# Performance work log

Measured on AMD Instinct MI355X. Metric: run time of the kernel, lower is better.

The kernel has to match this reference:

```python
import jax, jax.numpy as jnp
import numpy as np

B, S, D, H, DFF = 4, 2048, 1024, 8, 4096
DH = D // H  # 128
EPS = 1e-5


def layernorm(x, gamma, beta):
    mu = jnp.mean(x, axis=-1, keepdims=True)
    var = jnp.mean(jnp.square(x - mu), axis=-1, keepdims=True)
    return (x - mu) * jax.lax.rsqrt(var + EPS) * gamma + beta


def setup_inputs() -> dict:
    key = jax.random.key(0)
    ks = jax.random.split(key, 6)
    s = 0.02
    return {
        "src": jax.random.normal(ks[0], (B, S, D), jnp.float32),
        "w_qkv": jax.random.normal(ks[1], (D, 3 * D), jnp.float32) * s,
        "w_out": jax.random.normal(ks[2], (D, D), jnp.float32) * s,
        "w1": jax.random.normal(ks[3], (D, DFF), jnp.float32) * s,
        "b1": jnp.zeros((DFF,), jnp.float32),
        "w2": jax.random.normal(ks[4], (DFF, D), jnp.float32) * s,
        "b2": jnp.zeros((D,), jnp.float32),
        "g1": jnp.ones((D,), jnp.float32),
        "beta1": jnp.zeros((D,), jnp.float32),
        "g2": jnp.ones((D,), jnp.float32),
        "beta2": jnp.zeros((D,), jnp.float32),
    }


def reference(src, w_qkv, w_out, w1, b1, w2, b2, g1, beta1, g2, beta2):
    b, s, d = src.shape
    # --- RingAttention == exact causal MHA on a single device ---
    qkv = src @ w_qkv  # [b, s, 3d]
    q, k, v = jnp.split(qkv, 3, axis=-1)
    to_heads = lambda x: x.reshape(b, s, H, DH).transpose(0, 2, 1, 3)  # [b,h,s,dh]
    q, k, v = to_heads(q), to_heads(k), to_heads(v)
    scale = 1.0 / jnp.sqrt(jnp.asarray(DH, src.dtype))
    scores = jnp.einsum('bhqd,bhkd->bhqk', q, k) * scale  # [b,h,s,s]
    causal = jnp.tril(jnp.ones((s, s), bool))
    neg = jnp.asarray(jnp.finfo(src.dtype).min, src.dtype)
    scores = jnp.where(causal, scores, neg)
    attn = jax.nn.softmax(scores, axis=-1)
    o = jnp.einsum('bhqk,bhkd->bhqd', attn, v)  # [b,h,s,dh]
    o = o.transpose(0, 2, 1, 3).reshape(b, s, d) @ w_out
    # dropout layers are identity at inference
    x = layernorm(src + o, g1, beta1)
    ff = jax.nn.relu(x @ w1 + b1) @ w2 + b2
    return layernorm(x + ff, g2, beta2)
```

## Files before the change

### kernel.cpp

```cpp
#include <hip/hip_runtime.h>

typedef unsigned short u16;
typedef __attribute__((ext_vector_type(8))) short short8;
typedef __attribute__((ext_vector_type(4))) float float4v;

#define MFMA_BF16(a, b, c) __builtin_amdgcn_mfma_f32_16x16x32_bf16((a), (b), (c), 0, 0, 0)

#define B_ 4
#define S_ 2048
#define D_ 1024
#define H_ 8
#define DH_ 128
#define DFF_ 4096
#define EPS_ 1e-5f
#define ROWS_ (B_ * S_)
#define CSCALE_ 0.12751672939502f

__device__ __forceinline__ u16 f2bf(float f) {
  union { float f; unsigned u; } x; x.f = f;
  unsigned r = x.u + 0x7fffu + ((x.u >> 16) & 1u);
  return (u16)(r >> 16);
}

typedef __attribute__((address_space(1))) const unsigned int guint;
typedef __attribute__((address_space(3))) unsigned int luint;
__device__ __forceinline__ void gl2lds16(const u16* g, u16* l) {
  __builtin_amdgcn_global_load_lds((guint*)g, (luint*)l, 16, 0, 0);
}

__global__ void cast_bf16_kernel(const float* __restrict__ in, u16* __restrict__ out, int n4) {
  int i = blockIdx.x * blockDim.x + threadIdx.x;
  int stride = gridDim.x * blockDim.x;
  for (; i < n4; i += stride) {
    float4 v = ((const float4*)in)[i];
    ushort4 u;
    u.x = f2bf(v.x); u.y = f2bf(v.y); u.z = f2bf(v.z); u.w = f2bf(v.w);
    ((ushort4*)out)[i] = u;
  }
}

__global__ void transpose_cast_kernel(const float* __restrict__ in, u16* __restrict__ out,
                                      int K, int N) {
  __shared__ float t[32][33];
  int k0 = blockIdx.x * 32, n0 = blockIdx.y * 32;
  int tx = threadIdx.x & 31, ty = threadIdx.x >> 5;
  #pragma unroll
  for (int i = 0; i < 4; ++i)
    t[ty + 8 * i][tx] = in[(size_t)(k0 + ty + 8 * i) * N + n0 + tx];
  __syncthreads();
  #pragma unroll
  for (int i = 0; i < 4; ++i)
    out[(size_t)(n0 + ty + 8 * i) * K + k0 + tx] = f2bf(t[tx][ty + 8 * i]);
}

__global__ void transpose_v_kernel(const u16* __restrict__ in, u16* __restrict__ out) {
  __shared__ u16 t[32][33];
  int s0 = blockIdx.x * 32, d0 = blockIdx.y * 32, bh = blockIdx.z;
  const u16* src = in + (size_t)bh * S_ * DH_;
  u16* dst = out + (size_t)bh * DH_ * S_;
  int tx = threadIdx.x & 31, ty = threadIdx.x >> 5;
  #pragma unroll
  for (int i = 0; i < 4; ++i)
    t[ty + 8 * i][tx] = src[(size_t)(s0 + ty + 8 * i) * DH_ + d0 + tx];
  __syncthreads();
  #pragma unroll
  for (int i = 0; i < 4; ++i)
    dst[(size_t)(d0 + ty + 8 * i) * S_ + s0 + tx] = t[tx][ty + 8 * i];
}

template <int MODE, int KT>
__global__ __launch_bounds__(256) void gemm_kernel(
    const u16* __restrict__ A, const u16* __restrict__ Bt,
    const int M, const int N,
    float* __restrict__ outF, u16* __restrict__ outH, const float* __restrict__ bias,
    const float* __restrict__ resid,
    u16* __restrict__ qo, u16* __restrict__ ko, u16* __restrict__ vo) {
  __shared__ u16 As[2][128][32];
  __shared__ u16 Bs[2][128][32];
  const int tid = threadIdx.x;
  const int lane = tid & 63, wave = tid >> 6;
  const int quad = lane >> 4, r16 = lane & 15;
  const int wm = (wave >> 1) * 64, wn = (wave & 1) * 64;
  const int m0 = blockIdx.x * 128, n0 = blockIdx.y * 128;
  constexpr int K = KT, niter = KT >> 5;

  float4v acc[4][4];
  #pragma unroll
  for (int i = 0; i < 4; ++i)
    #pragma unroll
    for (int j = 0; j < 4; ++j) acc[i][j] = (float4v)0.0f;

  const int drow = lane >> 2;
  const int dchunk = (lane & 3) ^ ((drow ^ (drow >> 2)) & 3);
  const u16* Ag0 = A + (size_t)(m0 + wave * 32 + drow) * K + dchunk * 8;
  const u16* Ag1 = Ag0 + (size_t)16 * K;
  const u16* Bg0 = Bt + (size_t)(n0 + wave * 32 + drow) * K + dchunk * 8;
  const u16* Bg1 = Bg0 + (size_t)16 * K;
  u16* Al0 = &As[0][wave * 32][0];
  u16* Al1 = &As[0][wave * 32 + 16][0];
  u16* Bl0 = &Bs[0][wave * 32][0];
  u16* Bl1 = &Bs[0][wave * 32 + 16][0];
  constexpr int bufStep = 128 * 32;

  const int fcol = (quad ^ ((r16 ^ (r16 >> 2)) & 3)) * 8;

  gl2lds16(Ag0, Al0);
  gl2lds16(Ag1, Al1);
  gl2lds16(Bg0, Bl0);
  gl2lds16(Bg1, Bl1);

  #pragma unroll 2
  for (int i = 0; i < niter; ++i) {
    __syncthreads();
    if (i + 1 < niter) {
      const int k1 = (i + 1) << 5;
      const int bo = ((i + 1) & 1) ? bufStep : 0;
      gl2lds16(Ag0 + k1, Al0 + bo);
      gl2lds16(Ag1 + k1, Al1 + bo);
      gl2lds16(Bg0 + k1, Bl0 + bo);
      gl2lds16(Bg1 + k1, Bl1 + bo);
    }
    const u16* ab = &As[i & 1][0][0];
    const u16* bb = &Bs[i & 1][0][0];
    short8 af[4], bfv[4];
    #pragma unroll
    for (int t = 0; t < 4; ++t)
      af[t] = *(const short8*)(ab + ((wm + t * 16 + r16) << 5) + fcol);
    #pragma unroll
    for (int t = 0; t < 4; ++t)
      bfv[t] = *(const short8*)(bb + ((wn + t * 16 + r16) << 5) + fcol);
    #pragma unroll
    for (int ii = 0; ii < 4; ++ii)
      #pragma unroll
      for (int j = 0; j < 4; ++j) acc[ii][j] = MFMA_BF16(af[ii], bfv[j], acc[ii][j]);
  }

  #pragma unroll
  for (int i = 0; i < 4; ++i) {
    const int rowb = m0 + wm + i * 16 + quad * 4;
    #pragma unroll
    for (int j = 0; j < 4; ++j) {
      const int col = n0 + wn + j * 16 + r16;
      #pragma unroll
      for (int rg = 0; rg < 4; ++rg) {
        float val = acc[i][j][rg];
        const int r = rowb + rg;
        if (MODE == 0) {
          const int part = col >> 10, cc = col & 1023;
          const int h = cc >> 7, dh = cc & 127;
          const int b = r >> 11, s = r & 2047;
          u16* dst = (part == 0) ? qo : (part == 1) ? ko : vo;
          if (part == 0) val *= CSCALE_;
          dst[((size_t)(b * H_ + h) * S_ + s) * DH_ + dh] = f2bf(val);
        } else if (MODE == 1) {
          val += resid[(size_t)r * N + col];
          outF[(size_t)r * N + col] = val;
        } else if (MODE == 2) {
          val += bias[col];
          val = fmaxf(val, 0.0f);
          outH[(size_t)r * N + col] = f2bf(val);
        } else {
          val += bias[col] + resid[(size_t)r * N + col];
          outF[(size_t)r * N + col] = val;
        }
      }
    }
  }
}

__global__ __launch_bounds__(256) void attn_kernel(
    const u16* __restrict__ Q, const u16* __restrict__ Kg,
    const u16* __restrict__ Vtg, u16* __restrict__ O) {
  __shared__ u16 Ks[64][136];
  __shared__ u16 Vt[128][72];
  __shared__ u16 Pw[4][16][72];
  const int tid = threadIdx.x;
  const int lane = tid & 63, wave = tid >> 6;
  const int quad = lane >> 4, r16 = lane & 15;
  const int pairIdx = blockIdx.x;
  const int bh = blockIdx.y;
  const size_t base = (size_t)bh * S_ * DH_;
  const size_t vtb = (size_t)bh * DH_ * S_;
  const int b = bh >> 3, h = bh & 7;

  const u16* kg0 = Kg + base + (size_t)(tid >> 4) * DH_ + (tid & 15) * 8;
  u16* ksl = &Ks[tid >> 4][(tid & 15) * 8];
  const u16* vg0 = Vtg + vtb + (size_t)(tid >> 3) * S_ + (tid & 7) * 8;
  u16* vtl = &Vt[tid >> 3][(tid & 7) * 8];

  for (int half = 0; half < 2; ++half) {
    const int qb = (half == 0) ? pairIdx : 31 - pairIdx;
    const int qr = qb * 64 + wave * 16 + r16;

    short8 aq[4];
    #pragma unroll
    for (int ks = 0; ks < 4; ++ks)
      aq[ks] = *(const short8*)(Q + base + (size_t)qr * DH_ + ks * 32 + quad * 8);

    float4v acco[8];
    #pragma unroll
    for (int i = 0; i < 8; ++i) acco[i] = (float4v)0.0f;
    float m_q = -1e30f, l_q = 0.0f;

    for (int kb = 0; kb <= qb; ++kb) {
      __syncthreads();
      #pragma unroll
      for (int i = 0; i < 4; ++i)
        *(short8*)(ksl + i * 16 * 136) =
            *(const short8*)(kg0 + (size_t)(kb * 64 + i * 16) * DH_);
      #pragma unroll
      for (int i = 0; i < 4; ++i)
        *(short8*)(vtl + i * 32 * 72) =
            *(const short8*)(vg0 + (size_t)i * 32 * S_ + kb * 64);
      __syncthreads();

      float4v accs[4];
      #pragma unroll
      for (int t = 0; t < 4; ++t) accs[t] = (float4v)0.0f;
      #pragma unroll
      for (int ks = 0; ks < 4; ++ks) {
        #pragma unroll
        for (int t = 0; t < 4; ++t) {
          short8 ak = *(const short8*)&Ks[t * 16 + r16][ks * 32 + quad * 8];
          accs[t] = MFMA_BF16(ak, aq[ks], accs[t]);
        }
      }
      if (kb == qb) {
        #pragma unroll
        for (int t = 0; t < 4; ++t)
          #pragma unroll
          for (int rg = 0; rg < 4; ++rg) {
            int kc = kb * 64 + t * 16 + quad * 4 + rg;
            if (kc > qr) accs[t][rg] = -1e30f;
          }
      }
      float mv = accs[0][0];
      #pragma unroll
      for (int t = 0; t < 4; ++t)
        #pragma unroll
        for (int rg = 0; rg < 4; ++rg) mv = fmaxf(mv, accs[t][rg]);
      mv = fmaxf(mv, __shfl_xor(mv, 16));
      mv = fmaxf(mv, __shfl_xor(mv, 32));
      const float mnew = fmaxf(m_q, mv);
      const float alpha = __builtin_amdgcn_exp2f(m_q - mnew);
      float s0 = 0.0f;
      #pragma unroll
      for (int t = 0; t < 4; ++t)
        #pragma unroll
        for (int rg = 0; rg < 4; ++rg) {
          float p = __builtin_amdgcn_exp2f(accs[t][rg] - mnew);
          accs[t][rg] = p;
          s0 += p;
        }
      s0 += __shfl_xor(s0, 16);
      s0 += __shfl_xor(s0, 32);
      l_q = l_q * alpha + s0;
      m_q = mnew;

      #pragma unroll
      for (int t = 0; t < 4; ++t) {
        union { float f; unsigned u; } c0, c1, c2, c3;
        c0.f = accs[t][0]; c1.f = accs[t][1]; c2.f = accs[t][2]; c3.f = accs[t][3];
        uint2 pk;
        pk.x = ((c0.u + 0x8000u) >> 16) | ((c1.u + 0x8000u) & 0xffff0000u);
        pk.y = ((c2.u + 0x8000u) >> 16) | ((c3.u + 0x8000u) & 0xffff0000u);
        *(uint2*)&Pw[wave][r16][t * 16 + quad * 4] = pk;
      }
      float al[4];
      #pragma unroll
      for (int rg = 0; rg < 4; ++rg) al[rg] = __shfl(alpha, quad * 4 + rg);
      #pragma unroll
      for (int nt = 0; nt < 8; ++nt)
        #pragma unroll
        for (int rg = 0; rg < 4; ++rg) acco[nt][rg] *= al[rg];
      asm volatile("s_waitcnt lgkmcnt(0)" ::: "memory");
      #pragma unroll
      for (int ks2 = 0; ks2 < 2; ++ks2) {
        short8 ap = *(const short8*)&Pw[wave][r16][ks2 * 32 + quad * 8];
        #pragma unroll
        for (int nt = 0; nt < 8; ++nt) {
          short8 bv = *(const short8*)&Vt[nt * 16 + r16][ks2 * 32 + quad * 8];
          acco[nt] = MFMA_BF16(ap, bv, acco[nt]);
        }
      }
    }

    float lr[4];
    #pragma unroll
    for (int rg = 0; rg < 4; ++rg) lr[rg] = __shfl(l_q, quad * 4 + rg);
    const int sbase = qb * 64 + wave * 16 + quad * 4;
    #pragma unroll
    for (int nt = 0; nt < 8; ++nt)
      #pragma unroll
      for (int rg = 0; rg < 4; ++rg) {
        float val = acco[nt][rg] / lr[rg];
        O[((size_t)(b * S_ + sbase + rg)) * D_ + h * DH_ + nt * 16 + r16] = f2bf(val);
      }
  }
}

__global__ __launch_bounds__(256) void ln_kernel(
    const float* __restrict__ a,
    const float* __restrict__ g, const float* __restrict__ be,
    float* __restrict__ xf, u16* __restrict__ xb) {
  __shared__ float red[8];
  const int row = blockIdx.x, tid = threadIdx.x;
  float4 v = ((const float4*)(a + (size_t)row * D_))[tid];
  float s = v.x + v.y + v.z + v.w;
  float q = v.x * v.x + v.y * v.y + v.z * v.z + v.w * v.w;
  #pragma unroll
  for (int m = 1; m < 64; m <<= 1) {
    s += __shfl_xor(s, m);
    q += __shfl_xor(q, m);
  }
  const int wave = tid >> 6, lane = tid & 63;
  if (lane == 0) { red[wave] = s; red[4 + wave] = q; }
  __syncthreads();
  s = red[0] + red[1] + red[2] + red[3];
  q = red[4] + red[5] + red[6] + red[7];
  const float mu = s * (1.0f / D_);
  const float var = q * (1.0f / D_) - mu * mu;
  const float inv = rsqrtf(var + EPS_);
  const float4 gg = ((const float4*)g)[tid];
  const float4 bb = ((const float4*)be)[tid];
  float4 y;
  y.x = (v.x - mu) * inv * gg.x + bb.x;
  y.y = (v.y - mu) * inv * gg.y + bb.y;
  y.z = (v.z - mu) * inv * gg.z + bb.z;
  y.w = (v.w - mu) * inv * gg.w + bb.w;
  if (xf) ((float4*)(xf + (size_t)row * D_))[tid] = y;
  if (xb) {
    ushort4 u;
    u.x = f2bf(y.x); u.y = f2bf(y.y); u.z = f2bf(y.z); u.w = f2bf(y.w);
    ((ushort4*)(xb + (size_t)row * D_))[tid] = u;
  }
}

extern "C" void kernel_launch(void* const* d_in, const int* in_sizes, int n_in,
                              void* d_out, int out_size, void* d_ws, size_t ws_size,
                              hipStream_t stream) {
  const float* src   = (const float*)d_in[0];
  const float* w_qkv = (const float*)d_in[1];
  const float* w_out = (const float*)d_in[2];
  const float* w1    = (const float*)d_in[3];
  const float* b1    = (const float*)d_in[4];
  const float* w2    = (const float*)d_in[5];
  const float* b2    = (const float*)d_in[6];
  const float* g1    = (const float*)d_in[7];
  const float* be1   = (const float*)d_in[8];
  const float* g2    = (const float*)d_in[9];
  const float* be2   = (const float*)d_in[10];
  float* out = (float*)d_out;

  char* ws = (char*)d_ws;
  size_t off = 0;
  auto alloc = [&](size_t bytes) -> void* {
    void* p = ws + off;
    off += (bytes + 255) & ~(size_t)255;
    return p;
  };
  u16* src_bf = (u16*)alloc((size_t)ROWS_ * D_ * 2);
  u16* wqkvT  = (u16*)alloc((size_t)3 * D_ * D_ * 2);
  u16* woutT  = (u16*)alloc((size_t)D_ * D_ * 2);
  u16* w1T    = (u16*)alloc((size_t)DFF_ * D_ * 2);
  u16* w2T    = (u16*)alloc((size_t)D_ * DFF_ * 2);
  u16* qbuf   = (u16*)alloc((size_t)ROWS_ * D_ * 2);
  u16* kbuf   = (u16*)alloc((size_t)ROWS_ * D_ * 2);
  u16* vbuf   = (u16*)alloc((size_t)ROWS_ * D_ * 2);
  u16* obuf   = (u16*)alloc((size_t)ROWS_ * D_ * 2);
  u16* vT     = (u16*)alloc((size_t)ROWS_ * D_ * 2);
  float* proj = (float*)alloc((size_t)ROWS_ * D_ * 4);
  float* xf   = (float*)alloc((size_t)ROWS_ * D_ * 4);
  u16* xb     = (u16*)alloc((size_t)ROWS_ * D_ * 2);
  u16* h1     = qbuf;
  float* ff   = proj;

  cast_bf16_kernel<<<2048, 256, 0, stream>>>(src, src_bf, ROWS_ * D_ / 4);
  transpose_cast_kernel<<<dim3(D_ / 32, 3 * D_ / 32), 256, 0, stream>>>(w_qkv, wqkvT, D_, 3 * D_);
  transpose_cast_kernel<<<dim3(D_ / 32, D_ / 32), 256, 0, stream>>>(w_out, woutT, D_, D_);
  transpose_cast_kernel<<<dim3(D_ / 32, DFF_ / 32), 256, 0, stream>>>(w1, w1T, D_, DFF_);
  transpose_cast_kernel<<<dim3(DFF_ / 32, D_ / 32), 256, 0, stream>>>(w2, w2T, DFF_, D_);

  gemm_kernel<0, 1024><<<dim3(ROWS_ / 128, 3 * D_ / 128), 256, 0, stream>>>(
      src_bf, wqkvT, ROWS_, 3 * D_, nullptr, nullptr, nullptr, nullptr, qbuf, kbuf, vbuf);
  transpose_v_kernel<<<dim3(S_ / 32, DH_ / 32, B_ * H_), 256, 0, stream>>>(vbuf, vT);
  attn_kernel<<<dim3(16, B_ * H_), 256, 0, stream>>>(qbuf, kbuf, vT, obuf);
  gemm_kernel<1, 1024><<<dim3(ROWS_ / 128, D_ / 128), 256, 0, stream>>>(
      obuf, woutT, ROWS_, D_, proj, nullptr, nullptr, src, nullptr, nullptr, nullptr);
  ln_kernel<<<ROWS_, 256, 0, stream>>>(proj, g1, be1, xf, xb);
  gemm_kernel<2, 1024><<<dim3(ROWS_ / 128, DFF_ / 128), 256, 0, stream>>>(
      xb, w1T, ROWS_, DFF_, nullptr, h1, b1, nullptr, nullptr, nullptr, nullptr);
  gemm_kernel<3, 4096><<<dim3(ROWS_ / 128, D_ / 128), 256, 0, stream>>>(
      h1, w2T, ROWS_, D_, ff, nullptr, b2, xf, nullptr, nullptr, nullptr);
  ln_kernel<<<ROWS_, 256, 0, stream>>>(ff, g2, be2, out, nullptr);
}
```

Measured before the change: 557.6 us.

## Store GEMM A operands in 128x32 tiled layout and load fragments directly to registers

Every producer of a GEMM A operand (src cast, attention output, LayerNorm bf16 output, FFN1 output) now writes in a tiled 128x32 block layout. The GEMM then reads A fragments straight from global memory into registers, prefetching one k-step ahead, and drops the A shared-memory staging. This removes the A LDS traffic and its swizzle, at the cost of per-lane 16-byte global loads whose latency may not be hidden and of scattered stores in the producer kernels. A is no longer shared through LDS across the two waves that use the same rows, so each A tile is fetched from global or L2 twice.

```diff
diff --git a/kernel.cpp b/kernel.cpp
--- a/kernel.cpp
+++ b/kernel.cpp
@@ -28,15 +28,19 @@
   __builtin_amdgcn_global_load_lds((guint*)g, (luint*)l, 16, 0, 0);
 }
 
-__global__ void cast_bf16_kernel(const float* __restrict__ in, u16* __restrict__ out, int n4) {
-  int i = blockIdx.x * blockDim.x + threadIdx.x;
-  int stride = gridDim.x * blockDim.x;
-  for (; i < n4; i += stride) {
-    float4 v = ((const float4*)in)[i];
-    ushort4 u;
-    u.x = f2bf(v.x); u.y = f2bf(v.y); u.z = f2bf(v.z); u.w = f2bf(v.w);
-    ((ushort4*)out)[i] = u;
-  }
+__device__ __forceinline__ size_t tiled_off(int row, int k, int Kdim) {
+  return ((size_t)(row >> 7) * (Kdim >> 5) + (k >> 5)) * 4096 +
+         (size_t)((row & 127) << 5) + (k & 31);
+}
+
+__global__ void cast_tiled_kernel(const float* __restrict__ in, u16* __restrict__ out) {
+  int idx = blockIdx.x * 256 + threadIdx.x;
+  int g = idx * 4;
+  int m = g >> 10, k = g & 1023;
+  float4 v = *(const float4*)(in + (size_t)g);
+  ushort4 u;
+  u.x = f2bf(v.x); u.y = f2bf(v.y); u.z = f2bf(v.z); u.w = f2bf(v.w);
+  *(ushort4*)(out + tiled_off(m, k, D_)) = u;
 }
 
 __global__ void transpose_cast_kernel(const float* __restrict__ in, u16* __restrict__ out,
@@ -75,7 +79,6 @@
     float* __restrict__ outF, u16* __restrict__ outH, const float* __restrict__ bias,
     const float* __restrict__ resid,
     u16* __restrict__ qo, u16* __restrict__ ko, u16* __restrict__ vo) {
-  __shared__ u16 As[2][128][32];
   __shared__ u16 Bs[2][128][32];
   const int tid = threadIdx.x;
   const int lane = tid & 63, wave = tid >> 6;
@@ -90,24 +93,24 @@
     #pragma unroll
     for (int j = 0; j < 4; ++j) acc[i][j] = (float4v)0.0f;
 
-  const int drow = lane >> 2;
-  const int dchunk = (lane & 3) ^ ((drow ^ (drow >> 2)) & 3);
-  const u16* Ag0 = A + (size_t)(m0 + wave * 32 + drow) * K + dchunk * 8;
-  const u16* Ag1 = Ag0 + (size_t)16 * K;
-  const u16* Bg0 = Bt + (size_t)(n0 + wave * 32 + drow) * K + dchunk * 8;
+  const int drow = lane >> 2, dseg = lane & 3;
+  const u16* Bg0 = Bt + (size_t)(n0 + wave * 32 + drow) * K + dseg * 8;
   const u16* Bg1 = Bg0 + (size_t)16 * K;
-  u16* Al0 = &As[0][wave * 32][0];
-  u16* Al1 = &As[0][wave * 32 + 16][0];
   u16* Bl0 = &Bs[0][wave * 32][0];
   u16* Bl1 = &Bs[0][wave * 32 + 16][0];
   constexpr int bufStep = 128 * 32;
 
-  const int fcol = (quad ^ ((r16 ^ (r16 >> 2)) & 3)) * 8;
-
-  gl2lds16(Ag0, Al0);
-  gl2lds16(Ag1, Al1);
+  const u16* ap[4];
+  #pragma unroll
+  for (int t = 0; t < 4; ++t)
+    ap[t] = A + (size_t)(m0 >> 7) * niter * 4096 +
+            (size_t)((wm + t * 16 + r16) << 5) + quad * 8;
+
   gl2lds16(Bg0, Bl0);
   gl2lds16(Bg1, Bl1);
+  short8 a_cur[4], a_nxt[4];
+  #pragma unroll
+  for (int t = 0; t < 4; ++t) a_cur[t] = *(const short8*)(ap[t]);
 
   #pragma unroll 2
   for (int i = 0; i < niter; ++i) {
@@ -115,24 +118,22 @@
     if (i + 1 < niter) {
       const int k1 = (i + 1) << 5;
       const int bo = ((i + 1) & 1) ? bufStep : 0;
-      gl2lds16(Ag0 + k1, Al0 + bo);
-      gl2lds16(Ag1 + k1, Al1 + bo);
       gl2lds16(Bg0 + k1, Bl0 + bo);
       gl2lds16(Bg1 + k1, Bl1 + bo);
+      const size_t o = (size_t)(i + 1) * 4096;
+      #pragma unroll
+      for (int t = 0; t < 4; ++t) a_nxt[t] = *(const short8*)(ap[t] + o);
     }
-    const u16* ab = &As[i & 1][0][0];
-    const u16* bb = &Bs[i & 1][0][0];
-    short8 af[4], bfv[4];
+    short8 bfv[4];
     #pragma unroll
     for (int t = 0; t < 4; ++t)
-      af[t] = *(const short8*)(ab + ((wm + t * 16 + r16) << 5) + fcol);
-    #pragma unroll
-    for (int t = 0; t < 4; ++t)
-      bfv[t] = *(const short8*)(bb + ((wn + t * 16 + r16) << 5) + fcol);
+      bfv[t] = *(const short8*)&Bs[i & 1][wn + t * 16 + r16][quad * 8];
     #pragma unroll
     for (int ii = 0; ii < 4; ++ii)
       #pragma unroll
-      for (int j = 0; j < 4; ++j) acc[ii][j] = MFMA_BF16(af[ii], bfv[j], acc[ii][j]);
+      for (int j = 0; j < 4; ++j) acc[ii][j] = MFMA_BF16(a_cur[ii], bfv[j], acc[ii][j]);
+    #pragma unroll
+    for (int t = 0; t < 4; ++t) a_cur[t] = a_nxt[t];
   }
 
   #pragma unroll
@@ -158,7 +159,7 @@
         } else if (MODE == 2) {
           val += bias[col];
           val = fmaxf(val, 0.0f);
-          outH[(size_t)r * N + col] = f2bf(val);
+          outH[tiled_off(r, col, N)] = f2bf(val);
         } else {
           val += bias[col] + resid[(size_t)r * N + col];
           outF[(size_t)r * N + col] = val;
@@ -294,7 +295,9 @@
       #pragma unroll
       for (int rg = 0; rg < 4; ++rg) {
         float val = acco[nt][rg] / lr[rg];
-        O[((size_t)(b * S_ + sbase + rg)) * D_ + h * DH_ + nt * 16 + r16] = f2bf(val);
+        const int row = b * S_ + sbase + rg;
+        const int col = h * DH_ + nt * 16 + r16;
+        O[tiled_off(row, col, D_)] = f2bf(val);
       }
   }
 }
@@ -332,7 +335,7 @@
   if (xb) {
     ushort4 u;
     u.x = f2bf(y.x); u.y = f2bf(y.y); u.z = f2bf(y.z); u.w = f2bf(y.w);
-    ((ushort4*)(xb + (size_t)row * D_))[tid] = u;
+    *(ushort4*)(xb + tiled_off(row, tid * 4, D_)) = u;
   }
 }
 
@@ -375,7 +378,7 @@
   u16* h1     = qbuf;
   float* ff   = proj;
 
-  cast_bf16_kernel<<<2048, 256, 0, stream>>>(src, src_bf, ROWS_ * D_ / 4);
+  cast_tiled_kernel<<<ROWS_ * D_ / 4 / 256, 256, 0, stream>>>(src, src_bf);
   transpose_cast_kernel<<<dim3(D_ / 32, 3 * D_ / 32), 256, 0, stream>>>(w_qkv, wqkvT, D_, 3 * D_);
   transpose_cast_kernel<<<dim3(D_ / 32, D_ / 32), 256, 0, stream>>>(w_out, woutT, D_, D_);
   transpose_cast_kernel<<<dim3(D_ / 32, DFF_ / 32), 256, 0, stream>>>(w1, w1T, D_, DFF_);
```

Measured after the change: 555.1 us. Within noise of the previous version (-0.5%).
